# Kernel optimization log

Measured on AMD Instinct MI355X. Metric: run time of the kernel, lower is better.

The kernel has to match this reference:

```python
import jax, jax.numpy as jnp
import numpy as np

N_NODES = 50000
N_EDGES = 1600000
F_IN = 512      # 2 * embedding_dimension
HID = 512
OUT = 4
NEG_SLOPE = 0.01  # torch LeakyReLU default


def _leaky_relu(x):
    return jnp.where(x >= 0, x, NEG_SLOPE * x)


def setup_inputs() -> dict:
    key = jax.random.key(0)
    ks = jax.random.split(key, 12)
    s_in = 1.0 / np.sqrt(F_IN)
    s_h = 1.0 / np.sqrt(HID)
    return {
        "feature": jax.random.normal(ks[0], (N_NODES, F_IN), jnp.float32),
        "edge_index": jax.random.randint(ks[1], (2, N_EDGES), 0, N_NODES, jnp.int64),
        "edge_type": jax.random.randint(ks[2], (N_EDGES,), 0, 2, jnp.int64),
        # input MLP
        "W_in": jax.random.uniform(ks[3], (F_IN, HID), jnp.float32, -s_in, s_in),
        "b_in": jnp.zeros((HID,), jnp.float32),
        # sage1: lin_l (bias) on aggregated neighbors, lin_r (no bias) on self
        "W1_l": jax.random.uniform(ks[4], (HID, HID), jnp.float32, -s_h, s_h),
        "b1_l": jnp.zeros((HID,), jnp.float32),
        "W1_r": jax.random.uniform(ks[5], (HID, HID), jnp.float32, -s_h, s_h),
        # sage2
        "W2_l": jax.random.uniform(ks[6], (HID, HID), jnp.float32, -s_h, s_h),
        "b2_l": jnp.zeros((HID,), jnp.float32),
        "W2_r": jax.random.uniform(ks[7], (HID, HID), jnp.float32, -s_h, s_h),
        # output linear (hidden -> 4); note forward skips linear_relu_output1
        "W_out": jax.random.uniform(ks[8], (HID, OUT), jnp.float32, -s_h, s_h),
        "b_out": jnp.zeros((OUT,), jnp.float32),
    }


def _sage_conv(x, src, dst, W_l, b_l, W_r):
    # mean aggregation of source features onto destinations (PyG default flow)
    agg = jax.ops.segment_sum(x[src], dst, num_segments=N_NODES)  # [N, H]
    cnt = jax.ops.segment_sum(jnp.ones((src.shape[0], 1), x.dtype), dst,
                              num_segments=N_NODES)               # [N, 1]
    mean = agg / jnp.maximum(cnt, 1.0)
    return mean @ W_l + b_l + x @ W_r


def reference(feature, edge_index, edge_type,
              W_in, b_in, W1_l, b1_l, W1_r, W2_l, b2_l, W2_r, W_out, b_out):
    src, dst = edge_index[0], edge_index[1]
    x = _leaky_relu(feature.astype(jnp.float32) @ W_in + b_in)
    x = _sage_conv(x, src, dst, W1_l, b1_l, W1_r)
    # dropout is identity in eval mode
    x = _sage_conv(x, src, dst, W2_l, b2_l, W2_r)
    return x @ W_out + b_out
```

## Files before the change

kernel.cpp:

```cpp
#include <hip/hip_runtime.h>
#include <stdint.h>

#define NNODES 50000
#define NEDGES 1600000
#define HID 512
#define NEG_SLOPE 0.01f
#define NBUCK 98
#define NBLK 200
#define TILE 8000
#define NSUB 8
#define GPBLK 391
#define MROWS 50048

typedef __attribute__((ext_vector_type(8))) short bf16x8;
typedef __attribute__((ext_vector_type(8))) unsigned short u16x8;
typedef __attribute__((ext_vector_type(4))) float f32x4;

__device__ __forceinline__ float bf2f(unsigned short u) {
  unsigned int x = ((unsigned int)u) << 16;
  return __builtin_bit_cast(float, x);
}
__device__ __forceinline__ unsigned short f2bf(float f) {
  unsigned int u = __builtin_bit_cast(unsigned int, f);
  u += 0x7FFFu + ((u >> 16) & 1u);
  return (unsigned short)(u >> 16);
}
__device__ __forceinline__ void gload_lds16(const void* g, void* l) {
  __builtin_amdgcn_global_load_lds(
      (const __attribute__((address_space(1))) void*)g,
      (__attribute__((address_space(3))) void*)l, 16, 0, 0);
}

__global__ void flagk(const int* __restrict__ ei, int* __restrict__ flag) {
  int t = threadIdx.x;
  unsigned long long m = __ballot(ei[2 * t + 1] != 0);
  if (t == 0) *flag = (m != 0ULL) ? 1 : 0;
}

__global__ __launch_bounds__(256) void histk(const int* __restrict__ ei,
                                             const int* __restrict__ flag,
                                             int* __restrict__ hist) {
  __shared__ int h[NBUCK];
  int t = threadIdx.x, blk = blockIdx.x;
  for (int i = t; i < NBUCK; i += 256) h[i] = 0;
  __syncthreads();
  int f = *flag;
  int e0 = blk * TILE;
  for (int e = e0 + 2 * t; e < e0 + TILE; e += 512) {
    int d0, d1;
    if (f) {
      int2 v = *reinterpret_cast<const int2*>(&ei[(size_t)NEDGES + e]);
      d0 = v.x; d1 = v.y;
    } else {
      int4 v = *reinterpret_cast<const int4*>(&ei[2 * ((size_t)NEDGES + e)]);
      d0 = v.x; d1 = v.z;
    }
    if ((unsigned)d0 < NNODES) atomicAdd(&h[d0 >> 9], 1);
    if ((unsigned)d1 < NNODES) atomicAdd(&h[d1 >> 9], 1);
  }
  __syncthreads();
  for (int i = t; i < NBUCK; i += 256) hist[i * NBLK + blk] = h[i];
}

__global__ __launch_bounds__(512) void scanh(int* __restrict__ hist,
                                             int* __restrict__ bstart) {
  __shared__ int s[512];
  const int TOT = NBUCK * NBLK;
  const int C = 40;
  int t = threadIdx.x;
  int base = t * C;
  int sum = 0;
#pragma unroll
  for (int i = 0; i < C; i++) {
    int idx = base + i;
    sum += (idx < TOT) ? hist[idx] : 0;
  }
  s[t] = sum;
  __syncthreads();
  for (int off = 1; off < 512; off <<= 1) {
    int u = (t >= off) ? s[t - off] : 0;
    __syncthreads();
    s[t] += u;
    __syncthreads();
  }
  int run = (t > 0) ? s[t - 1] : 0;
#pragma unroll
  for (int i = 0; i < C; i++) {
    int idx = base + i;
    if (idx < TOT) {
      int v = hist[idx];
      hist[idx] = run;
      if (idx % NBLK == 0) bstart[idx / NBLK] = run;
      run += v;
    }
  }
  if (t == 511) bstart[NBUCK] = s[511];
}

__global__ __launch_bounds__(256) void binscatter(const int* __restrict__ ei,
                                                  const int* __restrict__ flag,
                                                  const int* __restrict__ hbase,
                                                  unsigned int* __restrict__ pcol) {
  __shared__ int lb[NBUCK];
  int t = threadIdx.x, blk = blockIdx.x;
  for (int i = t; i < NBUCK; i += 256) lb[i] = hbase[i * NBLK + blk];
  __syncthreads();
  int f = *flag;
  int e0 = blk * TILE;
  for (int e = e0 + 2 * t; e < e0 + TILE; e += 512) {
    int s0, s1, d0, d1;
    if (f) {
      int2 vs = *reinterpret_cast<const int2*>(&ei[e]);
      int2 vd = *reinterpret_cast<const int2*>(&ei[(size_t)NEDGES + e]);
      s0 = vs.x; s1 = vs.y; d0 = vd.x; d1 = vd.y;
    } else {
      int4 vs = *reinterpret_cast<const int4*>(&ei[2 * (size_t)e]);
      int4 vd = *reinterpret_cast<const int4*>(&ei[2 * ((size_t)NEDGES + e)]);
      s0 = vs.x; s1 = vs.z; d0 = vd.x; d1 = vd.z;
    }
    if ((unsigned)d0 < NNODES) {
      if ((unsigned)s0 >= NNODES) s0 = 0;
      int pos = atomicAdd(&lb[d0 >> 9], 1);
      pcol[pos] = ((unsigned)(d0 & 511) << 16) | (unsigned)s0;
    }
    if ((unsigned)d1 < NNODES) {
      if ((unsigned)s1 >= NNODES) s1 = 0;
      int pos = atomicAdd(&lb[d1 >> 9], 1);
      pcol[pos] = ((unsigned)(d1 & 511) << 16) | (unsigned)s1;
    }
  }
}

__global__ void tcast(const float* __restrict__ w, unsigned short* __restrict__ wt) {
  int i = blockIdx.x * 256 + threadIdx.x;
  int n = i >> 9, k = i & 511;
  wt[i] = f2bf(w[(k << 9) | n]);
}

__device__ __forceinline__ float wave_dot(const float* __restrict__ Arow,
                                          const float* __restrict__ B, int j) {
  int l = threadIdx.x & 63;
  float4 a0 = *reinterpret_cast<const float4*>(Arow + l * 8);
  float4 a1 = *reinterpret_cast<const float4*>(Arow + l * 8 + 4);
  const float* bb = B + (size_t)(l * 8) * 4 + j;
  float s = a0.x * bb[0] + a0.y * bb[4] + a0.z * bb[8] + a0.w * bb[12] +
            a1.x * bb[16] + a1.y * bb[20] + a1.z * bb[24] + a1.w * bb[28];
#pragma unroll
  for (int off = 1; off < 64; off <<= 1) s += __shfl_xor(s, off);
  return s;
}

__global__ __launch_bounds__(256) void smallA(
    const float* __restrict__ W2l, const float* __restrict__ W2r,
    const float* __restrict__ Wout, const float* __restrict__ b2l,
    const float* __restrict__ bout,
    float* __restrict__ Wlp, float* __restrict__ Wrp, float* __restrict__ bp) {
  int gw = blockIdx.x * 4 + (threadIdx.x >> 6);
  int l = threadIdx.x & 63;
  if (gw < 2048) {
    float v = wave_dot(W2l + (size_t)(gw >> 2) * 512, Wout, gw & 3);
    if (l == 0) Wlp[gw] = v;
  } else if (gw < 4096) {
    int g = gw - 2048;
    float v = wave_dot(W2r + (size_t)(g >> 2) * 512, Wout, g & 3);
    if (l == 0) Wrp[g] = v;
  } else if (gw < 4100) {
    int j = gw - 4096;
    float v = wave_dot(b2l, Wout, j);
    if (l == 0) bp[j] = v + bout[j];
  }
}

__global__ __launch_bounds__(256) void smallB(
    const float* __restrict__ W1l, const float* __restrict__ W1r,
    const float* __restrict__ b1l,
    const float* __restrict__ Wlp, const float* __restrict__ Wrp,
    const float* __restrict__ bp,
    float* __restrict__ Pall, float* __restrict__ kb, float* __restrict__ kc) {
  int gw = blockIdx.x * 4 + (threadIdx.x >> 6);
  int l = threadIdx.x & 63;
  if (gw < 6144) {
    int k = gw / 12, jg = gw % 12;
    int g = jg >> 2, j = jg & 3;
    float v;
    if (g == 0) v = wave_dot(W1l + (size_t)k * 512, Wlp, j);
    else if (g == 1) v = wave_dot(W1r + (size_t)k * 512, Wlp, j) +
                         wave_dot(W1l + (size_t)k * 512, Wrp, j);
    else v = wave_dot(W1r + (size_t)k * 512, Wrp, j);
    if (l == 0) Pall[k * 12 + jg] = v;
  } else if (gw < 6152) {
    int i = gw - 6144, j = i & 3;
    if (i < 4) {
      float v = wave_dot(b1l, Wlp, j);
      if (l == 0) kb[j] = v;
    } else {
      float v = wave_dot(b1l, Wrp, j);
      if (l == 0) kc[j] = v + bp[j];
    }
  }
}

__global__ __launch_bounds__(256) void gemmproj(
    const float* __restrict__ A, const unsigned short* __restrict__ Bt,
    const float* __restrict__ bias, const float* __restrict__ Pall,
    float* __restrict__ t0p) {
  __shared__ unsigned short As[128 * 32];
  __shared__ unsigned short Bs[128 * 32];
  __shared__ float tab[128 * 12];
  const int tid = threadIdx.x;
  const int wave = tid >> 6, lane = tid & 63;
  const int w = blockIdx.x;
  const int mt = (w & 7) + ((w >> 5) << 3);
  const int nb = (w >> 3) & 3;
  if (mt >= GPBLK) return;
  const int bm = mt * 128, bn = nb * 128;
  const int wr = wave >> 1, wc = wave & 1;
  const int r15 = lane & 15, kl = lane >> 4;
  const int srow = lane >> 2, soff = (lane & 3) * 8;

  for (int i = tid; i < 1536; i += 256) tab[i] = 0.f;

  f32x4 acc[4][4];
#pragma unroll
  for (int i = 0; i < 4; i++)
#pragma unroll
    for (int j = 0; j < 4; j++) acc[i][j] = {0.f, 0.f, 0.f, 0.f};

  for (int kt = 0; kt < HID / 32; ++kt) {
#pragma unroll
    for (int rr = 0; rr < 2; ++rr) {
      int c = wave * 2 + rr;
      int row = c * 16 + srow;
      gload_lds16(Bt + (size_t)(bn + row) * HID + kt * 32 + soff, (void*)&Bs[c * 512]);
    }
#pragma unroll
    for (int ss = 0; ss < 2; ++ss) {
      int s = tid + ss * 256;
      int row = s >> 2, k8 = (s & 3) * 8;
      int garow = bm + row;
      if (garow >= NNODES) garow = 0;
      const float* ga = A + (size_t)garow * HID + kt * 32 + k8;
      float4 v0 = *reinterpret_cast<const float4*>(ga);
      float4 v1 = *reinterpret_cast<const float4*>(ga + 4);
      u16x8 pk;
      pk[0] = f2bf(v0.x); pk[1] = f2bf(v0.y); pk[2] = f2bf(v0.z); pk[3] = f2bf(v0.w);
      pk[4] = f2bf(v1.x); pk[5] = f2bf(v1.y); pk[6] = f2bf(v1.z); pk[7] = f2bf(v1.w);
      *reinterpret_cast<u16x8*>(&As[row * 32 + k8]) = pk;
    }
    __syncthreads();
    bf16x8 af[4], bfr[4];
#pragma unroll
    for (int mi = 0; mi < 4; ++mi)
      af[mi] = *reinterpret_cast<const bf16x8*>(&As[(wr * 64 + mi * 16 + r15) * 32 + kl * 8]);
#pragma unroll
    for (int ni = 0; ni < 4; ++ni)
      bfr[ni] = *reinterpret_cast<const bf16x8*>(&Bs[(wc * 64 + ni * 16 + r15) * 32 + kl * 8]);
#pragma unroll
    for (int ni = 0; ni < 4; ++ni)
#pragma unroll
      for (int mi = 0; mi < 4; ++mi)
        acc[ni][mi] = __builtin_amdgcn_mfma_f32_16x16x32_bf16(bfr[ni], af[mi], acc[ni][mi], 0, 0, 0);
    __syncthreads();
  }

  float part[4][12];
#pragma unroll
  for (int mi = 0; mi < 4; ++mi)
#pragma unroll
    for (int j = 0; j < 12; ++j) part[mi][j] = 0.f;

#pragma unroll
  for (int ni = 0; ni < 4; ++ni) {
    int nbase = bn + wc * 64 + ni * 16 + kl * 4;
    float4 bv4 = *reinterpret_cast<const float4*>(bias + nbase);
    float bb[4] = {bv4.x, bv4.y, bv4.z, bv4.w};
#pragma unroll
    for (int rg = 0; rg < 4; ++rg) {
      const float* Pc = Pall + (size_t)(nbase + rg) * 12;
      float4 p0 = *reinterpret_cast<const float4*>(Pc);
      float4 p1 = *reinterpret_cast<const float4*>(Pc + 4);
      float4 p2 = *reinterpret_cast<const float4*>(Pc + 8);
#pragma unroll
      for (int mi = 0; mi < 4; ++mi) {
        float v = acc[ni][mi][rg] + bb[rg];
        v = (v >= 0.f) ? v : NEG_SLOPE * v;
        part[mi][0] += v * p0.x; part[mi][1] += v * p0.y;
        part[mi][2] += v * p0.z; part[mi][3] += v * p0.w;
        part[mi][4] += v * p1.x; part[mi][5] += v * p1.y;
        part[mi][6] += v * p1.z; part[mi][7] += v * p1.w;
        part[mi][8] += v * p2.x; part[mi][9] += v * p2.y;
        part[mi][10] += v * p2.z; part[mi][11] += v * p2.w;
      }
    }
  }
#pragma unroll
  for (int mi = 0; mi < 4; ++mi)
#pragma unroll
    for (int j = 0; j < 12; ++j) {
      part[mi][j] += __shfl_xor(part[mi][j], 16);
      part[mi][j] += __shfl_xor(part[mi][j], 32);
    }
  if (kl == 0) {
#pragma unroll
    for (int mi = 0; mi < 4; ++mi) {
      int r = wr * 64 + mi * 16 + r15;
#pragma unroll
      for (int j = 0; j < 12; ++j) atomicAdd(&tab[r * 12 + j], part[mi][j]);
    }
  }
  __syncthreads();
  float* o = t0p + (size_t)nb * MROWS * 12 + (size_t)bm * 12;
  for (int i = tid; i < 1536; i += 256) o[i] = tab[i];
}

__global__ __launch_bounds__(256) void reduce_t0(const float* __restrict__ t0p,
                                                 float* __restrict__ t0) {
  int i = blockIdx.x * 256 + threadIdx.x;
  if (i >= NNODES * 12) return;
  const size_t S = (size_t)MROWS * 12;
  t0[i] = t0p[i] + t0p[S + i] + t0p[2 * S + i] + t0p[3 * S + i];
}

__global__ __launch_bounds__(256) void aggA(
    const unsigned int* __restrict__ pcol, const int* __restrict__ bstart,
    const float* __restrict__ t0, float* __restrict__ partial) {
  __shared__ float tab[512 * 5];
  int t = threadIdx.x;
  int b = blockIdx.x >> 3, sb = blockIdx.x & 7;
  for (int i = t; i < 2560; i += 256) tab[i] = 0.f;
  __syncthreads();
  int st = bstart[b], en = bstart[b + 1];
  int len = en - st;
  int a0 = st + (int)(((long long)len * sb) >> 3);
  int a1 = st + (int)(((long long)len * (sb + 1)) >> 3);
  for (int e = a0 + t; e < a1; e += 256) {
    unsigned v = pcol[e];
    int i = v >> 16, src = v & 0xFFFF;
    float4 x = *reinterpret_cast<const float4*>(t0 + (size_t)src * 12);
    atomicAdd(&tab[i * 5 + 0], x.x);
    atomicAdd(&tab[i * 5 + 1], x.y);
    atomicAdd(&tab[i * 5 + 2], x.z);
    atomicAdd(&tab[i * 5 + 3], x.w);
    atomicAdd(&tab[i * 5 + 4], 1.f);
  }
  __syncthreads();
  float* o = partial + (size_t)blockIdx.x * 2560;
  for (int i = t; i < 2560; i += 256) o[i] = tab[i];
}

__global__ __launch_bounds__(256) void finA(
    const float* __restrict__ partial, const float* __restrict__ t0,
    float* __restrict__ s1, float* __restrict__ degf) {
  int n = blockIdx.x * 256 + threadIdx.x;
  if (n >= NNODES) return;
  int b = n >> 9, i = n & 511;
  float a[5] = {0.f, 0.f, 0.f, 0.f, 0.f};
#pragma unroll
  for (int s = 0; s < 8; s++) {
    const float* p = partial + (size_t)(b * 8 + s) * 2560 + i * 5;
#pragma unroll
    for (int j = 0; j < 5; j++) a[j] += p[j];
  }
  float deg = a[4];
  float sc = (deg > 0.f) ? 1.f / deg : 0.f;
  float4 tb = *reinterpret_cast<const float4*>(t0 + (size_t)n * 12 + 4);
  float4 o = {a[0] * sc + tb.x, a[1] * sc + tb.y, a[2] * sc + tb.z, a[3] * sc + tb.w};
  *reinterpret_cast<float4*>(s1 + (size_t)n * 4) = o;
  degf[n] = deg;
}

__global__ __launch_bounds__(256) void aggB(
    const unsigned int* __restrict__ pcol, const int* __restrict__ bstart,
    const float* __restrict__ s1, float* __restrict__ partial) {
  __shared__ float tab[512 * 4];
  int t = threadIdx.x;
  int b = blockIdx.x >> 3, sb = blockIdx.x & 7;
  for (int i = t; i < 2048; i += 256) tab[i] = 0.f;
  __syncthreads();
  int st = bstart[b], en = bstart[b + 1];
  int len = en - st;
  int a0 = st + (int)(((long long)len * sb) >> 3);
  int a1 = st + (int)(((long long)len * (sb + 1)) >> 3);
  for (int e = a0 + t; e < a1; e += 256) {
    unsigned v = pcol[e];
    int i = v >> 16, src = v & 0xFFFF;
    float4 x = *reinterpret_cast<const float4*>(s1 + (size_t)src * 4);
    atomicAdd(&tab[i * 4 + 0], x.x);
    atomicAdd(&tab[i * 4 + 1], x.y);
    atomicAdd(&tab[i * 4 + 2], x.z);
    atomicAdd(&tab[i * 4 + 3], x.w);
  }
  __syncthreads();
  float* o = partial + (size_t)blockIdx.x * 2048;
  for (int i = t; i < 2048; i += 256) o[i] = tab[i];
}

__global__ __launch_bounds__(256) void finB(
    const float* __restrict__ partial, const float* __restrict__ t0,
    const float* __restrict__ degf, const float* __restrict__ kb,
    const float* __restrict__ kc, float* __restrict__ out) {
  int n = blockIdx.x * 256 + threadIdx.x;
  if (n >= NNODES) return;
  int b = n >> 9, i = n & 511;
  float a[4] = {0.f, 0.f, 0.f, 0.f};
#pragma unroll
  for (int s = 0; s < 8; s++) {
    const float* p = partial + (size_t)(b * 8 + s) * 2048 + i * 4;
#pragma unroll
    for (int j = 0; j < 4; j++) a[j] += p[j];
  }
  float deg = degf[n];
  float sc = (deg > 0.f) ? 1.f / deg : 0.f;
  float ind = (deg > 0.f) ? 1.f : 0.f;
  float4 c = *reinterpret_cast<const float4*>(t0 + (size_t)n * 12 + 8);
  float4 vb = *reinterpret_cast<const float4*>(kb);
  float4 vc = *reinterpret_cast<const float4*>(kc);
  float4 o = {a[0] * sc + c.x + ind * vb.x + vc.x,
              a[1] * sc + c.y + ind * vb.y + vc.y,
              a[2] * sc + c.z + ind * vb.z + vc.z,
              a[3] * sc + c.w + ind * vb.w + vc.w};
  *reinterpret_cast<float4*>(out + (size_t)n * 4) = o;
}

extern "C" void kernel_launch(void* const* d_in, const int* in_sizes, int n_in,
                              void* d_out, int out_size, void* d_ws, size_t ws_size,
                              hipStream_t stream) {
  const float* feat = (const float*)d_in[0];
  const int* ei = (const int*)d_in[1];
  const float* W_in = (const float*)d_in[3];
  const float* b_in = (const float*)d_in[4];
  const float* W1l = (const float*)d_in[5];
  const float* b1l = (const float*)d_in[6];
  const float* W1r = (const float*)d_in[7];
  const float* W2l = (const float*)d_in[8];
  const float* b2l = (const float*)d_in[9];
  const float* W2r = (const float*)d_in[10];
  const float* Wout = (const float*)d_in[11];
  const float* bout = (const float*)d_in[12];
  float* out = (float*)d_out;

  char* ws = (char*)d_ws;
  size_t off = 0;
  auto alloc = [&](size_t bytes) {
    void* p = ws + off;
    off += (bytes + 15) & ~(size_t)15;
    return p;
  };
  int* flag   = (int*)alloc(16);
  int* hist   = (int*)alloc((size_t)NBUCK * NBLK * 4);
  int* bstart = (int*)alloc((NBUCK + 1) * 4);
  unsigned int* pcol = (unsigned int*)alloc((size_t)NEDGES * 4);
  unsigned short* Wt0 = (unsigned short*)alloc(512 * 512 * 2);
  float* Wlp  = (float*)alloc(2048 * 4);
  float* Wrp  = (float*)alloc(2048 * 4);
  float* bp   = (float*)alloc(16);
  float* Pall = (float*)alloc(512 * 12 * 4);
  float* kb   = (float*)alloc(16);
  float* kc   = (float*)alloc(16);
  float* t0   = (float*)alloc((size_t)NNODES * 12 * 4);
  float* t0p  = (float*)alloc((size_t)4 * MROWS * 12 * 4);
  float* s1   = (float*)alloc((size_t)NNODES * 4 * 4);
  float* degf = (float*)alloc((size_t)NNODES * 4);
  float* partial = (float*)alloc((size_t)NBUCK * NSUB * 2560 * 4);
  (void)ws_size;

  flagk<<<1, 64, 0, stream>>>(ei, flag);
  histk<<<NBLK, 256, 0, stream>>>(ei, flag, hist);
  scanh<<<1, 512, 0, stream>>>(hist, bstart);
  binscatter<<<NBLK, 256, 0, stream>>>(ei, flag, hist, pcol);

  tcast<<<1024, 256, 0, stream>>>(W_in, Wt0);
  smallA<<<1025, 256, 0, stream>>>(W2l, W2r, Wout, b2l, bout, Wlp, Wrp, bp);
  smallB<<<1538, 256, 0, stream>>>(W1l, W1r, b1l, Wlp, Wrp, bp, Pall, kb, kc);

  gemmproj<<<1568, 256, 0, stream>>>(feat, Wt0, b_in, Pall, t0p);
  reduce_t0<<<(NNODES * 12 + 255) / 256, 256, 0, stream>>>(t0p, t0);
  aggA<<<NBUCK * NSUB, 256, 0, stream>>>(pcol, bstart, t0, partial);
  finA<<<(NNODES + 255) / 256, 256, 0, stream>>>(partial, t0, s1, degf);
  aggB<<<NBUCK * NSUB, 256, 0, stream>>>(pcol, bstart, s1, partial);
  finB<<<(NNODES + 255) / 256, 256, 0, stream>>>(partial, t0, degf, kb, kc, out);
}
```

Baseline: 306.2 us.

## Precast features to bf16 and load GEMM A tiles via direct global-to-LDS

Adds a separate pass that converts the fp32 feature matrix to a zero-padded bf16 buffer once. The projection GEMM then loads A tiles with the same direct global-to-LDS path as B, removing the per-tile fp32 loads and in-register conversion. The epilogue is reordered to keep fewer partial sums live, and a launch bound requesting 4 blocks per CU is added for occupancy. The trade is an extra full read and write of the feature matrix. Since the 4 column blocks each re-read A, the GEMM's own A traffic is halved.

```diff
diff --git a/kernel.cpp b/kernel.cpp
--- a/kernel.cpp
+++ b/kernel.cpp
@@ -129,6 +129,24 @@
       pcol[pos] = ((unsigned)(d1 & 511) << 16) | (unsigned)s1;
     }
   }
+}
+
+__global__ __launch_bounds__(256) void castA(const float* __restrict__ f,
+                                             unsigned short* __restrict__ o) {
+  int idx = blockIdx.x * 256 + threadIdx.x;
+  if (idx >= MROWS * 64) return;
+  size_t g = (size_t)idx * 8;
+  int row = idx >> 6;
+  u16x8 pk;
+  if (row < NNODES) {
+    float4 v0 = *reinterpret_cast<const float4*>(f + g);
+    float4 v1 = *reinterpret_cast<const float4*>(f + g + 4);
+    pk[0] = f2bf(v0.x); pk[1] = f2bf(v0.y); pk[2] = f2bf(v0.z); pk[3] = f2bf(v0.w);
+    pk[4] = f2bf(v1.x); pk[5] = f2bf(v1.y); pk[6] = f2bf(v1.z); pk[7] = f2bf(v1.w);
+  } else {
+    pk = (u16x8)0;
+  }
+  *reinterpret_cast<u16x8*>(o + g) = pk;
 }
 
 __global__ void tcast(const float* __restrict__ w, unsigned short* __restrict__ wt) {
@@ -200,8 +218,8 @@
   }
 }
 
-__global__ __launch_bounds__(256) void gemmproj(
-    const float* __restrict__ A, const unsigned short* __restrict__ Bt,
+__global__ __launch_bounds__(256, 4) void gemmproj(
+    const unsigned short* __restrict__ Ab, const unsigned short* __restrict__ Bt,
     const float* __restrict__ bias, const float* __restrict__ Pall,
     float* __restrict__ t0p) {
   __shared__ unsigned short As[128 * 32];
@@ -231,21 +249,8 @@
     for (int rr = 0; rr < 2; ++rr) {
       int c = wave * 2 + rr;
       int row = c * 16 + srow;
+      gload_lds16(Ab + (size_t)(bm + row) * HID + kt * 32 + soff, (void*)&As[c * 512]);
       gload_lds16(Bt + (size_t)(bn + row) * HID + kt * 32 + soff, (void*)&Bs[c * 512]);
-    }
-#pragma unroll
-    for (int ss = 0; ss < 2; ++ss) {
-      int s = tid + ss * 256;
-      int row = s >> 2, k8 = (s & 3) * 8;
-      int garow = bm + row;
-      if (garow >= NNODES) garow = 0;
-      const float* ga = A + (size_t)garow * HID + kt * 32 + k8;
-      float4 v0 = *reinterpret_cast<const float4*>(ga);
-      float4 v1 = *reinterpret_cast<const float4*>(ga + 4);
-      u16x8 pk;
-      pk[0] = f2bf(v0.x); pk[1] = f2bf(v0.y); pk[2] = f2bf(v0.z); pk[3] = f2bf(v0.w);
-      pk[4] = f2bf(v1.x); pk[5] = f2bf(v1.y); pk[6] = f2bf(v1.z); pk[7] = f2bf(v1.w);
-      *reinterpret_cast<u16x8*>(&As[row * 32 + k8]) = pk;
     }
     __syncthreads();
     bf16x8 af[4], bfr[4];
@@ -263,49 +268,38 @@
     __syncthreads();
   }
 
-  float part[4][12];
-#pragma unroll
-  for (int mi = 0; mi < 4; ++mi)
-#pragma unroll
-    for (int j = 0; j < 12; ++j) part[mi][j] = 0.f;
-
-#pragma unroll
-  for (int ni = 0; ni < 4; ++ni) {
-    int nbase = bn + wc * 64 + ni * 16 + kl * 4;
-    float4 bv4 = *reinterpret_cast<const float4*>(bias + nbase);
-    float bb[4] = {bv4.x, bv4.y, bv4.z, bv4.w};
-#pragma unroll
-    for (int rg = 0; rg < 4; ++rg) {
-      const float* Pc = Pall + (size_t)(nbase + rg) * 12;
-      float4 p0 = *reinterpret_cast<const float4*>(Pc);
-      float4 p1 = *reinterpret_cast<const float4*>(Pc + 4);
-      float4 p2 = *reinterpret_cast<const float4*>(Pc + 8);
-#pragma unroll
-      for (int mi = 0; mi < 4; ++mi) {
+#pragma unroll
+  for (int mi = 0; mi < 4; ++mi) {
+    float p12[12];
+#pragma unroll
+    for (int j = 0; j < 12; ++j) p12[j] = 0.f;
+#pragma unroll
+    for (int ni = 0; ni < 4; ++ni) {
+      int nbase = bn + wc * 64 + ni * 16 + kl * 4;
+      float4 bv4 = *reinterpret_cast<const float4*>(bias + nbase);
+      float bb[4] = {bv4.x, bv4.y, bv4.z, bv4.w};
+#pragma unroll
+      for (int rg = 0; rg < 4; ++rg) {
         float v = acc[ni][mi][rg] + bb[rg];
         v = (v >= 0.f) ? v : NEG_SLOPE * v;
-        part[mi][0] += v * p0.x; part[mi][1] += v * p0.y;
-        part[mi][2] += v * p0.z; part[mi][3] += v * p0.w;
-        part[mi][4] += v * p1.x; part[mi][5] += v * p1.y;
-        part[mi][6] += v * p1.z; part[mi][7] += v * p1.w;
-        part[mi][8] += v * p2.x; part[mi][9] += v * p2.y;
-        part[mi][10] += v * p2.z; part[mi][11] += v * p2.w;
+        const float* Pc = Pall + (size_t)(nbase + rg) * 12;
+        float4 p0 = *reinterpret_cast<const float4*>(Pc);
+        float4 p1 = *reinterpret_cast<const float4*>(Pc + 4);
+        float4 p2 = *reinterpret_cast<const float4*>(Pc + 8);
+        p12[0] += v * p0.x; p12[1] += v * p0.y; p12[2] += v * p0.z; p12[3] += v * p0.w;
+        p12[4] += v * p1.x; p12[5] += v * p1.y; p12[6] += v * p1.z; p12[7] += v * p1.w;
+        p12[8] += v * p2.x; p12[9] += v * p2.y; p12[10] += v * p2.z; p12[11] += v * p2.w;
       }
     }
-  }
-#pragma unroll
-  for (int mi = 0; mi < 4; ++mi)
 #pragma unroll
     for (int j = 0; j < 12; ++j) {
-      part[mi][j] += __shfl_xor(part[mi][j], 16);
-      part[mi][j] += __shfl_xor(part[mi][j], 32);
-    }
-  if (kl == 0) {
-#pragma unroll
-    for (int mi = 0; mi < 4; ++mi) {
+      p12[j] += __shfl_xor(p12[j], 16);
+      p12[j] += __shfl_xor(p12[j], 32);
+    }
+    if (kl == 0) {
       int r = wr * 64 + mi * 16 + r15;
 #pragma unroll
-      for (int j = 0; j < 12; ++j) atomicAdd(&tab[r * 12 + j], part[mi][j]);
+      for (int j = 0; j < 12; ++j) atomicAdd(&tab[r * 12 + j], p12[j]);
     }
   }
   __syncthreads();
@@ -450,6 +444,7 @@
   int* hist   = (int*)alloc((size_t)NBUCK * NBLK * 4);
   int* bstart = (int*)alloc((NBUCK + 1) * 4);
   unsigned int* pcol = (unsigned int*)alloc((size_t)NEDGES * 4);
+  unsigned short* featb = (unsigned short*)alloc((size_t)MROWS * HID * 2);
   unsigned short* Wt0 = (unsigned short*)alloc(512 * 512 * 2);
   float* Wlp  = (float*)alloc(2048 * 4);
   float* Wrp  = (float*)alloc(2048 * 4);
@@ -469,11 +464,12 @@
   scanh<<<1, 512, 0, stream>>>(hist, bstart);
   binscatter<<<NBLK, 256, 0, stream>>>(ei, flag, hist, pcol);
 
+  castA<<<(MROWS * 64 + 255) / 256, 256, 0, stream>>>(feat, featb);
   tcast<<<1024, 256, 0, stream>>>(W_in, Wt0);
   smallA<<<1025, 256, 0, stream>>>(W2l, W2r, Wout, b2l, bout, Wlp, Wrp, bp);
   smallB<<<1538, 256, 0, stream>>>(W1l, W1r, b1l, Wlp, Wrp, bp, Pall, kb, kc);
 
-  gemmproj<<<1568, 256, 0, stream>>>(feat, Wt0, b_in, Pall, t0p);
+  gemmproj<<<1568, 256, 0, stream>>>(featb, Wt0, b_in, Pall, t0p);
   reduce_t0<<<(NNODES * 12 + 255) / 256, 256, 0, stream>>>(t0p, t0);
   aggA<<<NBUCK * NSUB, 256, 0, stream>>>(pcol, bstart, t0, partial);
   finA<<<(NNODES + 255) / 256, 256, 0, stream>>>(partial, t0, s1, degf);
```

Measured after the change: 303.7 us. No clear change (-0.8%).
